# Performance work log

Hardware: AMD Instinct MI355X
Metric: run time of the kernel (lower is better)

Reference implementation:

```python
import jax, jax.numpy as jnp
import numpy as np

DIM = 512
A_HEADS = 8
C_HEADS = 4
DH = 64
EPS = 1e-5


def layer_norm(x, g, b):
    mu = jnp.mean(x, axis=-1, keepdims=True)
    var = jnp.var(x, axis=-1, keepdims=True)
    return (x - mu) * jax.lax.rsqrt(var + EPS) * g + b


def setup_inputs() -> dict:
    key = jax.random.key(0)
    ks = jax.random.split(key, 8)
    inner_a = A_HEADS * DH  # 512
    inner_c = C_HEADS * DH  # 256
    s = 0.02
    return {
        "x": jax.random.normal(ks[0], (4, 192, DIM), dtype=jnp.float32),
        # Attention branch params
        "ln1_g": jnp.ones((DIM,), jnp.float32),
        "ln1_b": jnp.zeros((DIM,), jnp.float32),
        "Wqkv": jax.random.normal(ks[1], (DIM, 3 * inner_a), jnp.float32) * s,
        "Wo": jax.random.normal(ks[2], (inner_a, DIM), jnp.float32) * s,
        "bo": jnp.zeros((DIM,), jnp.float32),
        # Trittention branch params
        "ln2_g": jnp.ones((DIM,), jnp.float32),
        "ln2_b": jnp.zeros((DIM,), jnp.float32),
        "Wabcde": jax.random.normal(ks[3], (DIM, 5 * inner_c), jnp.float32) * s,
        "babcde": jnp.zeros((5 * inner_c,), jnp.float32),
        "Wp": jax.random.normal(ks[4], (inner_c, DIM), jnp.float32) * s,
        "bp": jnp.zeros((DIM,), jnp.float32),
    }


def _attention(x, ln_g, ln_b, Wqkv, Wo, bo):
    B, T, _ = x.shape
    xn = layer_norm(x, ln_g, ln_b)
    qkv = xn @ Wqkv  # [B,T,3*H*D]
    q, k, v = jnp.split(qkv, 3, axis=-1)
    def heads(t):
        return t.reshape(B, T, A_HEADS, DH).transpose(0, 2, 1, 3)  # [B,H,T,D]
    q, k, v = heads(q), heads(k), heads(v)
    scale = DH ** -0.5
    dots = jnp.einsum('bhqd,bhkd->bhqk', q, k) * scale
    attn = jax.nn.softmax(dots, axis=-1)
    out = jnp.einsum('bhqk,bhkd->bhqd', attn, v)
    out = out.transpose(0, 2, 1, 3).reshape(B, T, A_HEADS * DH)
    return out @ Wo + bo


def _trittention(x, ln_g, ln_b, Wabcde, babcde, Wp, bp):
    B, T, _ = x.shape
    xn = layer_norm(x, ln_g, ln_b)
    proj = xn @ Wabcde + babcde  # [B,T,5*H*D]
    a, b_, c, d_, e = jnp.split(proj, 5, axis=-1)
    def heads(t):
        return t.reshape(B, T, C_HEADS, DH)  # [B,T,H,D]
    a, b_, c, d_, e = heads(a), heads(b_), heads(c), heads(d_), heads(e)
    # cubic score: [B,H,S,T,Q]
    score = jnp.einsum('bshd,bthd,bqhd->bhstq', a, b_, c) / DH
    # softmax over joint (s,t) for each query q
    score = score.transpose(0, 1, 4, 2, 3).reshape(B, C_HEADS, T, T * T)
    attn = jax.nn.softmax(score, axis=-1).reshape(B, C_HEADS, T, T, T)
    z = (jnp.einsum('bhqst,bshd->bhqd', attn, d_)
         + jnp.einsum('bhqst,bthd->bhqd', attn, e))
    z = z.transpose(0, 2, 1, 3).reshape(B, T, C_HEADS * DH)
    return z @ Wp + bp


def reference(x, ln1_g, ln1_b, Wqkv, Wo, bo, ln2_g, ln2_b, Wabcde, babcde, Wp, bp):
    return (_attention(x, ln1_g, ln1_b, Wqkv, Wo, bo)
            + _trittention(x, ln2_g, ln2_b, Wabcde, babcde, Wp, bp))
```

## Files before the change

kernel.cpp:

```cpp
#include <hip/hip_runtime.h>
#include <cstdint>


#define B_   4
#define T_   192
#define DIM_ 512
#define AH   8
#define CH   4

typedef unsigned short u16;
typedef unsigned int   u32;
typedef __attribute__((ext_vector_type(8))) short short8;
typedef __attribute__((ext_vector_type(4))) float floatx4;
typedef __attribute__((ext_vector_type(4))) int intx4;
typedef __attribute__((ext_vector_type(2))) float f32x2;
typedef __attribute__((ext_vector_type(8))) _Float16 half8;
typedef __attribute__((ext_vector_type(2))) _Float16 half2v;
typedef __attribute__((ext_vector_type(2))) __fp16 fp16x2;

union Frag  { intx4 i; short8 s; };
union FragH { intx4 i; half8 h; };

__device__ __forceinline__ floatx4 mfma16(Frag a, Frag b, floatx4 c) {
    return __builtin_amdgcn_mfma_f32_16x16x32_bf16(a.s, b.s, c, 0, 0, 0);
}
__device__ __forceinline__ floatx4 mfma16h(FragH a, FragH b, floatx4 c) {
    return __builtin_amdgcn_mfma_f32_16x16x32_f16(a.h, b.h, c, 0, 0, 0);
}

__device__ __forceinline__ float fexp2(float x) {
    return __builtin_amdgcn_exp2f(x);
}

__device__ __forceinline__ float wave_reduce_sum(float v) {
#pragma unroll
    for (int off = 32; off >= 1; off >>= 1)
        v += __shfl_xor(v, off, 64);
    return v;
}

__device__ __forceinline__ u32 pack_rne(float x, float y) {
    u32 ux = __float_as_uint(x);
    u32 uy = __float_as_uint(y);
    ux += 0x7fffu + ((ux >> 16) & 1u);
    uy += 0x7fffu + ((uy >> 16) & 1u);
    return (ux >> 16) | (uy & 0xffff0000u);
}
__device__ __forceinline__ u16 bf16_rne(float x) {
    u32 u = __float_as_uint(x);
    u += 0x7fffu + ((u >> 16) & 1u);
    return (u16)(u >> 16);
}
__device__ __forceinline__ float bf16f(u16 h) { return __uint_as_float(((u32)h) << 16); }

__device__ __forceinline__ u32 pack_f16(float x, float y) {
    union { fp16x2 h; u32 u; } cv;
    cv.h = __builtin_amdgcn_cvt_pkrtz(x, y);
    return cv.u;
}
__device__ __forceinline__ u32 mul_h2(u32 a, u32 b) {
    union { u32 u; half2v h; } ua, ub, uw;
    ua.u = a; ub.u = b;
    uw.h = ua.h * ub.h;
    return uw.u;
}

__device__ __forceinline__ Frag ld_frag8(const u16* p) {
    Frag f;
    uint2 a = *(const uint2*)p;
    uint2 b = *(const uint2*)(p + 4);
    f.i = (intx4){ (int)a.x, (int)a.y, (int)b.x, (int)b.y };
    return f;
}

#define LOG2E 1.44269504088896f

__global__ __launch_bounds__(256) void prep_kernel(
    const float* __restrict__ x,
    const float* __restrict__ g1, const float* __restrict__ b1,
    const float* __restrict__ g2, const float* __restrict__ b2,
    u16* __restrict__ x1h, u16* __restrict__ x2h,
    const float* __restrict__ Wqkv, u16* __restrict__ wqh,
    const float* __restrict__ Wab,  u16* __restrict__ wah,
    const float* __restrict__ Wo,   const float* __restrict__ Wp,
    u16* __restrict__ wofh, float* __restrict__ zero_base, float* __restrict__ outz)
{
    __shared__ union { float t[64][65]; float red[4][2]; } u;
    const int tid = threadIdx.x;
    {
        int gid = blockIdx.x * 256 + tid;
        if (gid < 294912) ((float4*)zero_base)[gid] = make_float4(0.f, 0.f, 0.f, 0.f);
        if (gid < 98304)  ((float4*)outz)[gid]      = make_float4(0.f, 0.f, 0.f, 0.f);
    }
    if (blockIdx.x < 768) {
        int row = blockIdx.x;
        const float2 v = ((const float2*)(x + (size_t)row * DIM_))[tid];
        float s  = v.x + v.y;
        float s2 = v.x * v.x + v.y * v.y;
        s  = wave_reduce_sum(s);
        s2 = wave_reduce_sum(s2);
        int w = tid >> 6;
        if ((tid & 63) == 0) { u.red[w][0] = s; u.red[w][1] = s2; }
        __syncthreads();
        float ts  = u.red[0][0] + u.red[1][0] + u.red[2][0] + u.red[3][0];
        float ts2 = u.red[0][1] + u.red[1][1] + u.red[2][1] + u.red[3][1];
        float mean = ts * (1.0f / DIM_);
        float var  = ts2 * (1.0f / DIM_) - mean * mean;
        float rstd = rsqrtf(var + 1e-5f);
        int c0 = tid * 2;
        float n0 = (v.x - mean) * rstd;
        float n1 = (v.y - mean) * rstd;
        float a0 = n0 * g1[c0] + b1[c0], a1 = n1 * g1[c0 + 1] + b1[c0 + 1];
        float c2 = n0 * g2[c0] + b2[c0], c3 = n1 * g2[c0 + 1] + b2[c0 + 1];
        size_t o = (size_t)row * 256 + tid;
        ((u32*)x1h)[o] = pack_rne(a0, a1);
        ((u32*)x2h)[o] = pack_rne(c2, c3);
        return;
    }
    int id = blockIdx.x - 768;
    const float* W; u16 *H; int K, N, Kout, kofs, tile;
    if (id < 192)      { W = Wqkv; H = wqh;  K = 512; N = 1536; Kout = 512; kofs = 0;   tile = id;       }
    else if (id < 352) { W = Wab;  H = wah;  K = 512; N = 1280; Kout = 512; kofs = 0;   tile = id - 192; }
    else if (id < 416) { W = Wo;   H = wofh; K = 512; N = 512;  Kout = 768; kofs = 0;   tile = id - 352; }
    else               { W = Wp;   H = wofh; K = 256; N = 512;  Kout = 768; kofs = 512; tile = id - 416; }
    int nx = N >> 6;
    int n0 = (tile % nx) * 64, k0 = (tile / nx) * 64;
    int rr = tid >> 4, c4 = (tid & 15) << 2;
#pragma unroll
    for (int p = 0; p < 4; ++p) {
        int row = rr + p * 16;
        float4 v = *(const float4*)(W + (size_t)(k0 + row) * N + n0 + c4);
        u.t[row][c4 + 0] = v.x; u.t[row][c4 + 1] = v.y;
        u.t[row][c4 + 2] = v.z; u.t[row][c4 + 3] = v.w;
    }
    __syncthreads();
#pragma unroll
    for (int p = 0; p < 4; ++p) {
        int n = rr + p * 16;
        u16 hi[4];
#pragma unroll
        for (int c = 0; c < 4; ++c)
            hi[c] = bf16_rne(u.t[c4 + c][n]);
        size_t o = (size_t)(n0 + n) * Kout + kofs + k0 + c4;
        *(uint2*)&H[o] = make_uint2((u32)hi[0] | ((u32)hi[1] << 16), (u32)hi[2] | ((u32)hi[3] << 16));
    }
}

__global__ __launch_bounds__(256) void gemm_dual(
    const u16* __restrict__ x1h, const u16* __restrict__ wqh,
    const u16* __restrict__ x2h, const u16* __restrict__ wah,
    const float* __restrict__ babcde,
    float* __restrict__ qkv, float* __restrict__ proj)
{
    __shared__ u16 As[64][68];
    __shared__ u16 Bs[64][68];
    const int tid = threadIdx.x;
    const int nb = blockIdx.x;
    const u16 *Ah, *BTh; const float* bias; float* C; int N, bn;
    if (nb < 24) { Ah = x1h; BTh = wqh; bias = nullptr; C = qkv;  N = 1536; bn = nb * 64; }
    else         { Ah = x2h; BTh = wah; bias = babcde; C = proj; N = 1280; bn = (nb - 24) * 64; }
    const int K = 512;
    const int bm = blockIdx.y * 64;
    const int lane = tid & 63, wave = tid >> 6;
    const int m16 = lane & 15, quad = lane >> 4;
    const int wm = (wave >> 1) * 32, wn = (wave & 1) * 32;
    const int r = tid >> 2, c16 = (tid & 3) * 16;

    floatx4 acc[2][2];
#pragma unroll
    for (int i = 0; i < 2; ++i)
#pragma unroll
        for (int j = 0; j < 2; ++j) acc[i][j] = (floatx4){0.f, 0.f, 0.f, 0.f};

    for (int k0 = 0; k0 < K; k0 += 64) {
        __syncthreads();
        {
            const u16* pa = Ah + (size_t)(bm + r) * K + k0 + c16;
            uint4 v0 = *(const uint4*)pa, v1 = *(const uint4*)(pa + 8);
            *(uint2*)&As[r][c16 + 0]  = make_uint2(v0.x, v0.y);
            *(uint2*)&As[r][c16 + 4]  = make_uint2(v0.z, v0.w);
            *(uint2*)&As[r][c16 + 8]  = make_uint2(v1.x, v1.y);
            *(uint2*)&As[r][c16 + 12] = make_uint2(v1.z, v1.w);
        }
        {
            const u16* pb = BTh + (size_t)(bn + r) * K + k0 + c16;
            uint4 v0 = *(const uint4*)pb, v1 = *(const uint4*)(pb + 8);
            *(uint2*)&Bs[r][c16 + 0]  = make_uint2(v0.x, v0.y);
            *(uint2*)&Bs[r][c16 + 4]  = make_uint2(v0.z, v0.w);
            *(uint2*)&Bs[r][c16 + 8]  = make_uint2(v1.x, v1.y);
            *(uint2*)&Bs[r][c16 + 12] = make_uint2(v1.z, v1.w);
        }
        __syncthreads();
#pragma unroll
        for (int ks = 0; ks < 2; ++ks) {
            const int ko = ks * 32 + quad * 8;
            Frag a0 = ld_frag8(&As[wm + m16][ko]);
            Frag a1 = ld_frag8(&As[wm + 16 + m16][ko]);
            Frag b0 = ld_frag8(&Bs[wn + m16][ko]);
            Frag b1 = ld_frag8(&Bs[wn + 16 + m16][ko]);
            acc[0][0] = mfma16(a0, b0, acc[0][0]);
            acc[0][1] = mfma16(a0, b1, acc[0][1]);
            acc[1][0] = mfma16(a1, b0, acc[1][0]);
            acc[1][1] = mfma16(a1, b1, acc[1][1]);
        }
    }
#pragma unroll
    for (int i = 0; i < 2; ++i)
#pragma unroll
        for (int rr = 0; rr < 4; ++rr) {
            int m = bm + wm + i * 16 + quad * 4 + rr;
#pragma unroll
            for (int j = 0; j < 2; ++j) {
                int n = bn + wn + j * 16 + m16;
                float v = acc[i][j][rr];
                if (bias) v += bias[n];
                C[(size_t)m * N + n] = v;
            }
        }
}

__global__ __launch_bounds__(256, 3) void attn_tritt(
    const float* __restrict__ qkv, const float* __restrict__ proj,
    u16* __restrict__ aoh, float* __restrict__ rs1, float* __restrict__ rt1)
{
    __shared__ union {
        struct {
            union { u16 Ks[96][68]; u16 P[64][100]; } kp;
            u16 Vt[64][100];
        } at;
        struct {
            u32 a_lds[48 * 36];
            u32 b_lds[48 * 36];
            float rs_lds[48][33];
            float rt_lds[48][33];
        } tr;
    } S;
    const int tid = threadIdx.x;
    const int lane = tid & 63, wave = tid >> 6;
    const int m16 = lane & 15, quad = lane >> 4;

    if (blockIdx.x < 96) {
        const int ab = blockIdx.x;
        const int b = ab / 24, rem = ab % 24;
        const int h = rem / 3, qt3 = rem % 3;
        const int qg = wave;
        const size_t base = (size_t)(b * T_) * 1536 + h * 64;

        Frag qf0, qf1;
        {
            const float s = 0.125f * LOG2E;
            const float* qp = qkv + base + (size_t)(qt3 * 64 + qg * 16 + m16) * 1536 + quad * 8;
            float4 u0 = *(const float4*)qp;
            float4 u1 = *(const float4*)(qp + 4);
            float4 u2 = *(const float4*)(qp + 32);
            float4 u3 = *(const float4*)(qp + 36);
            qf0.i = (intx4){ (int)pack_rne(u0.x * s, u0.y * s), (int)pack_rne(u0.z * s, u0.w * s),
                             (int)pack_rne(u1.x * s, u1.y * s), (int)pack_rne(u1.z * s, u1.w * s) };
            qf1.i = (intx4){ (int)pack_rne(u2.x * s, u2.y * s), (int)pack_rne(u2.z * s, u2.w * s),
                             (int)pack_rne(u3.x * s, u3.y * s), (int)pack_rne(u3.z * s, u3.w * s) };
        }

        float rsum[4] = {0.f, 0.f, 0.f, 0.f};
        floatx4 acco[4];
#pragma unroll
        for (int dt = 0; dt < 4; ++dt) acco[dt] = (floatx4){0.f, 0.f, 0.f, 0.f};

        for (int p = 0; p < 2; ++p) {
            if (p) __syncthreads();
            for (int i = tid; i < 96 * 16; i += 256) {
                int row = i >> 4, c4 = (i & 15) << 2;
                const float* kp = qkv + base + (size_t)(p * 96 + row) * 1536 + 512 + c4;
                float4 kv = *(const float4*)kp;
                *(uint2*)&S.at.kp.Ks[row][c4] = make_uint2(pack_rne(kv.x, kv.y), pack_rne(kv.z, kv.w));
                float4 vv = *(const float4*)(qkv + base + (size_t)(p * 96 + row) * 1536 + 1024 + c4);
                S.at.Vt[c4 + 0][row] = bf16_rne(vv.x);
                S.at.Vt[c4 + 1][row] = bf16_rne(vv.y);
                S.at.Vt[c4 + 2][row] = bf16_rne(vv.z);
                S.at.Vt[c4 + 3][row] = bf16_rne(vv.w);
            }
            __syncthreads();

            float ev[6][4];
#pragma unroll
            for (int tt = 0; tt < 6; ++tt) {
                Frag kb0 = ld_frag8(&S.at.kp.Ks[tt * 16 + m16][quad * 8]);
                Frag kb1 = ld_frag8(&S.at.kp.Ks[tt * 16 + m16][32 + quad * 8]);
                floatx4 accs = (floatx4){0.f, 0.f, 0.f, 0.f};
                accs = mfma16(qf0, kb0, accs);
                accs = mfma16(qf1, kb1, accs);
#pragma unroll
                for (int rr = 0; rr < 4; ++rr) {
                    float e = fexp2(accs[rr]);
                    ev[tt][rr] = e;
                    rsum[rr] += e;
                }
            }
            __syncthreads();
#pragma unroll
            for (int tt = 0; tt < 6; ++tt)
#pragma unroll
                for (int rr = 0; rr < 4; ++rr)
                    S.at.kp.P[qg * 16 + quad * 4 + rr][tt * 16 + m16] = bf16_rne(ev[tt][rr]);
#pragma unroll
            for (int ts = 0; ts < 3; ++ts) {
                Frag pf = ld_frag8(&S.at.kp.P[qg * 16 + m16][ts * 32 + quad * 8]);
#pragma unroll
                for (int dt = 0; dt < 4; ++dt) {
                    Frag vf = ld_frag8(&S.at.Vt[dt * 16 + m16][ts * 32 + quad * 8]);
                    acco[dt] = mfma16(pf, vf, acco[dt]);
                }
            }
        }

        float rinv[4];
#pragma unroll
        for (int rr = 0; rr < 4; ++rr) {
            float v = rsum[rr];
            v += __shfl_xor(v, 1, 64);
            v += __shfl_xor(v, 2, 64);
            v += __shfl_xor(v, 4, 64);
            v += __shfl_xor(v, 8, 64);
            rinv[rr] = 1.0f / v;
        }
#pragma unroll
        for (int dt = 0; dt < 4; ++dt)
#pragma unroll
            for (int rr = 0; rr < 4; ++rr) {
                float o = acco[dt][rr] * rinv[rr];
                size_t idx = (size_t)(b * T_ + qt3 * 64 + qg * 16 + quad * 4 + rr) * 512
                           + h * 64 + dt * 16 + m16;
                aoh[idx] = bf16_rne(o);
            }
        return;
    }

    const int t2 = blockIdx.x - 96;
    const int xx = t2 % 96;
    const int h = (t2 / 96) % CH;
    const int b = t2 / (96 * CH);
    const int qt = xx >> 4;
    const int sc = (xx >> 2) & 3;
    const int tc = xx & 3;
    const int q0 = qt * 32, s0 = sc * 48, t0 = tc * 48;
    const int bh = b * CH + h;
    const size_t rowbase = (size_t)(b * T_) * 1280 + h * 64;
    const float kA = 0.015625f * LOG2E;

    for (int i = tid; i < 48 * 32; i += 256) {
        int row = i >> 5, cp = i & 31;
        const float2 va = *(const float2*)(proj + rowbase + (size_t)(s0 + row) * 1280 + 0 + cp * 2);
        S.tr.a_lds[row * 36 + cp] = pack_f16(va.x * kA, va.y * kA);
        const float2 vb = *(const float2*)(proj + rowbase + (size_t)(t0 + row) * 1280 + 256 + cp * 2);
        S.tr.b_lds[row * 36 + cp] = pack_f16(vb.x, vb.y);
    }

    FragH cf[2][2];
#pragma unroll
    for (int jq = 0; jq < 2; ++jq) {
        const float* cp = proj + rowbase + (size_t)(q0 + jq * 16 + m16) * 1280 + 512 + quad * 8;
        float4 u0 = *(const float4*)(cp);
        float4 u1 = *(const float4*)(cp + 4);
        float4 u2 = *(const float4*)(cp + 32);
        float4 u3 = *(const float4*)(cp + 36);
        cf[jq][0].i = (intx4){ (int)pack_f16(u0.x, u0.y), (int)pack_f16(u0.z, u0.w),
                               (int)pack_f16(u1.x, u1.y), (int)pack_f16(u1.z, u1.w) };
        cf[jq][1].i = (intx4){ (int)pack_f16(u2.x, u2.y), (int)pack_f16(u2.z, u2.w),
                               (int)pack_f16(u3.x, u3.y), (int)pack_f16(u3.z, u3.w) };
    }
    __syncthreads();

    float rt_acc[3][4][2] = {};

    for (int si = 0; si < 12; ++si) {
        const int srow = wave * 12 + si;
        const intx4 av0 = *(const intx4*)(S.tr.a_lds + srow * 36 + quad * 4);
        const intx4 av1 = *(const intx4*)(S.tr.a_lds + srow * 36 + 16 + quad * 4);
        float rs_s[2] = {0.f, 0.f};
#pragma unroll
        for (int tt = 0; tt < 3; ++tt) {
            const u32* bp2 = S.tr.b_lds + (tt * 16 + m16) * 36;
            intx4 bv0 = *(const intx4*)(bp2 + quad * 4);
            intx4 bv1 = *(const intx4*)(bp2 + 16 + quad * 4);
            FragH w0, w1;
#pragma unroll
            for (int j = 0; j < 4; ++j) {
                w0.i[j] = (int)mul_h2((u32)av0[j], (u32)bv0[j]);
                w1.i[j] = (int)mul_h2((u32)av1[j], (u32)bv1[j]);
            }
#pragma unroll
            for (int jq = 0; jq < 2; ++jq) {
                floatx4 acc = (floatx4){0.f, 0.f, 0.f, 0.f};
                acc = mfma16h(w0, cf[jq][0], acc);
                acc = mfma16h(w1, cf[jq][1], acc);
#pragma unroll
                for (int rr = 0; rr < 4; ++rr) {
                    float e = fexp2(acc[rr]);
                    rt_acc[tt][rr][jq] += e;
                    rs_s[jq] += e;
                }
            }
        }
#pragma unroll
        for (int jq = 0; jq < 2; ++jq) {
            float v = rs_s[jq];
            v += __shfl_xor(v, 16, 64);
            v += __shfl_xor(v, 32, 64);
            if (lane < 16) S.tr.rs_lds[srow][jq * 16 + m16] = v;
        }
    }

    __syncthreads();
    for (int w = 0; w < 4; ++w) {
        if (wave == w) {
#pragma unroll
            for (int tt = 0; tt < 3; ++tt)
#pragma unroll
                for (int rr = 0; rr < 4; ++rr) {
                    int t = tt * 16 + quad * 4 + rr;
#pragma unroll
                    for (int jq = 0; jq < 2; ++jq) {
                        if (w == 0) S.tr.rt_lds[t][jq * 16 + m16] = rt_acc[tt][rr][jq];
                        else        S.tr.rt_lds[t][jq * 16 + m16] += rt_acc[tt][rr][jq];
                    }
                }
        }
        __syncthreads();
    }
    for (int i = tid; i < 32 * 48; i += 256) {
        int qq = i / 48, ss = i - qq * 48;
        unsafeAtomicAdd(&rs1[((size_t)bh * T_ + q0 + qq) * T_ + s0 + ss], S.tr.rs_lds[ss][qq]);
    }
    for (int i = tid; i < 32 * 48; i += 256) {
        int qq = i / 48, t3 = i - qq * 48;
        unsafeAtomicAdd(&rt1[((size_t)bh * T_ + q0 + qq) * T_ + t0 + t3], S.tr.rt_lds[t3][qq]);
    }
}

__global__ __launch_bounds__(256) void finale(
    const u16* __restrict__ aoh, const float* __restrict__ rs1, const float* __restrict__ rt1,
    const float* __restrict__ proj, const u16* __restrict__ wofh,
    const float* __restrict__ bo, const float* __restrict__ bp,
    float* __restrict__ out)
{
    __shared__ union {
        struct { u16 As[32][68]; u16 Bs[64][68]; } A;
        struct { u16 Am[2][32][68]; u16 Bs[64][68]; float zred[32][9]; float Zl[32]; } B;
    } S;
    const int tid = threadIdx.x;
    const int lane = tid & 63, wave = tid >> 6;
    const int m16 = lane & 15, quad = lane >> 4;

    if (blockIdx.x < 192) {
        const int bn = (blockIdx.x & 7) * 64, bm = (blockIdx.x >> 3) * 32;
        const int wm = (wave >> 1) * 16, wn = (wave & 1) * 32;
        const int ra = tid >> 3, c8 = (tid & 7) * 8;
        const int rb = tid >> 2, c16 = (tid & 3) * 16;

        floatx4 acc[2];
        acc[0] = (floatx4){0.f, 0.f, 0.f, 0.f};
        acc[1] = (floatx4){0.f, 0.f, 0.f, 0.f};

        for (int k0 = 0; k0 < 512; k0 += 64) {
            __syncthreads();
            {
                const u16* pah = aoh + (size_t)(bm + ra) * 512 + k0 + c8;
                uint4 v = *(const uint4*)pah;
                *(uint2*)&S.A.As[ra][c8 + 0] = make_uint2(v.x, v.y);
                *(uint2*)&S.A.As[ra][c8 + 4] = make_uint2(v.z, v.w);
            }
            {
                const u16* pb = wofh + (size_t)(bn + rb) * 768 + k0 + c16;
                uint4 v0 = *(const uint4*)pb, v1 = *(const uint4*)(pb + 8);
                *(uint2*)&S.A.Bs[rb][c16 + 0]  = make_uint2(v0.x, v0.y);
                *(uint2*)&S.A.Bs[rb][c16 + 4]  = make_uint2(v0.z, v0.w);
                *(uint2*)&S.A.Bs[rb][c16 + 8]  = make_uint2(v1.x, v1.y);
                *(uint2*)&S.A.Bs[rb][c16 + 12] = make_uint2(v1.z, v1.w);
            }
            __syncthreads();
#pragma unroll
            for (int ks = 0; ks < 2; ++ks) {
                const int ko = ks * 32 + quad * 8;
                Frag ah = ld_frag8(&S.A.As[wm + m16][ko]);
                Frag b0 = ld_frag8(&S.A.Bs[wn + m16][ko]);
                Frag b1 = ld_frag8(&S.A.Bs[wn + 16 + m16][ko]);
                acc[0] = mfma16(ah, b0, acc[0]);
                acc[1] = mfma16(ah, b1, acc[1]);
            }
        }
#pragma unroll
        for (int rr = 0; rr < 4; ++rr) {
            int m = bm + wm + quad * 4 + rr;
#pragma unroll
            for (int j = 0; j < 2; ++j) {
                int n = bn + wn + j * 16 + m16;
                unsafeAtomicAdd(&out[(size_t)m * 512 + n], acc[j][rr] + bo[n] + bp[n]);
            }
        }
        return;
    }

    const int blockB = blockIdx.x - 192;
    const int mt = blockB % 6, bh = blockB / 6;
    const int b = bh >> 2, h = bh & 3;
    const int q0 = mt * 32;
    const int wm = (wave >> 1) * 16, wn = (wave & 1) * 32;
    const int ra = tid >> 3, c8 = (tid & 7) * 8;
    const int sl = tid >> 2, d4b = (tid & 3) * 4;

    float zacc = 0.f;
    floatx4 acc[2];
    acc[0] = (floatx4){0.f, 0.f, 0.f, 0.f};
    acc[1] = (floatx4){0.f, 0.f, 0.f, 0.f};

    for (int k0 = 0; k0 < 384; k0 += 64) {
        __syncthreads();
        {
            float g[8];
            if (k0 < 192) {
                const float* p = rs1 + ((size_t)bh * T_ + q0 + ra) * T_ + k0 + c8;
                float4 v0 = *(const float4*)(p);
                float4 v1 = *(const float4*)(p + 4);
                g[0] = v0.x; g[1] = v0.y; g[2] = v0.z; g[3] = v0.w;
                g[4] = v1.x; g[5] = v1.y; g[6] = v1.z; g[7] = v1.w;
                zacc += ((g[0] + g[1]) + (g[2] + g[3])) + ((g[4] + g[5]) + (g[6] + g[7]));
            } else {
                const float* p = rt1 + ((size_t)bh * T_ + q0 + ra) * T_ + (k0 - 192) + c8;
                float4 v0 = *(const float4*)(p);
                float4 v1 = *(const float4*)(p + 4);
                g[0] = v0.x; g[1] = v0.y; g[2] = v0.z; g[3] = v0.w;
                g[4] = v1.x; g[5] = v1.y; g[6] = v1.z; g[7] = v1.w;
            }
#pragma unroll
            for (int i = 0; i < 8; ++i) {
                u16 hi = bf16_rne(g[i]);
                S.B.Am[0][ra][c8 + i] = hi;
                S.B.Am[1][ra][c8 + i] = bf16_rne(g[i] - bf16f(hi));
            }
        }
        {
            const int colbase = (k0 < 192 ? 768 : 1024) + h * 64;
            const int s0 = (k0 < 192 ? k0 : k0 - 192);
#pragma unroll
            for (int i = 0; i < 4; ++i) {
                int dd = d4b + i * 16;
                float4 v = *(const float4*)(proj + (size_t)(b * T_ + s0 + sl) * 1280 + colbase + dd);
                S.B.Bs[dd + 0][sl] = bf16_rne(v.x);
                S.B.Bs[dd + 1][sl] = bf16_rne(v.y);
                S.B.Bs[dd + 2][sl] = bf16_rne(v.z);
                S.B.Bs[dd + 3][sl] = bf16_rne(v.w);
            }
        }
        __syncthreads();
#pragma unroll
        for (int ks = 0; ks < 2; ++ks) {
            const int ko = ks * 32 + quad * 8;
            Frag gh = ld_frag8(&S.B.Am[0][wm + m16][ko]);
            Frag gl = ld_frag8(&S.B.Am[1][wm + m16][ko]);
            Frag d0 = ld_frag8(&S.B.Bs[wn + m16][ko]);
            Frag d1 = ld_frag8(&S.B.Bs[wn + 16 + m16][ko]);
            acc[0] = mfma16(gh, d0, acc[0]);
            acc[0] = mfma16(gl, d0, acc[0]);
            acc[1] = mfma16(gh, d1, acc[1]);
            acc[1] = mfma16(gl, d1, acc[1]);
        }
    }
    S.B.zred[ra][tid & 7] = zacc;
    __syncthreads();
    if (tid < 32) {
        float s = ((S.B.zred[tid][0] + S.B.zred[tid][1]) + (S.B.zred[tid][2] + S.B.zred[tid][3]))
                + ((S.B.zred[tid][4] + S.B.zred[tid][5]) + (S.B.zred[tid][6] + S.B.zred[tid][7]));
        S.B.Zl[tid] = 1.0f / s;
    }
    __syncthreads();
    {
        float zv[2][4];
#pragma unroll
        for (int j = 0; j < 2; ++j)
#pragma unroll
            for (int rr = 0; rr < 4; ++rr) {
                int m = wm + quad * 4 + rr;
                zv[j][rr] = acc[j][rr] * S.B.Zl[m];
            }
        __syncthreads();
#pragma unroll
        for (int j = 0; j < 2; ++j)
#pragma unroll
            for (int rr = 0; rr < 4; ++rr) {
                int m = wm + quad * 4 + rr;
                int d = wn + j * 16 + m16;
                S.B.Am[0][m][d] = bf16_rne(zv[j][rr]);
            }
    }
    __syncthreads();
#pragma unroll
    for (int t = 0; t < 8; ++t) {
        const int n0 = wave * 128 + t * 16;
        Frag bf0 = ld_frag8(&wofh[(size_t)(n0 + m16) * 768 + 512 + h * 64 + quad * 8]);
        Frag bf1 = ld_frag8(&wofh[(size_t)(n0 + m16) * 768 + 512 + h * 64 + 32 + quad * 8]);
#pragma unroll
        for (int qi = 0; qi < 2; ++qi) {
            Frag za = ld_frag8(&S.B.Am[0][qi * 16 + m16][quad * 8]);
            Frag zb = ld_frag8(&S.B.Am[0][qi * 16 + m16][32 + quad * 8]);
            floatx4 ac = (floatx4){0.f, 0.f, 0.f, 0.f};
            ac = mfma16(za, bf0, ac);
            ac = mfma16(zb, bf1, ac);
#pragma unroll
            for (int rr = 0; rr < 4; ++rr) {
                int m = b * T_ + q0 + qi * 16 + quad * 4 + rr;
                unsafeAtomicAdd(&out[(size_t)m * 512 + n0 + m16], ac[rr]);
            }
        }
    }
}

extern "C" void kernel_launch(void* const* d_in, const int* in_sizes, int n_in,
                              void* d_out, int out_size, void* d_ws, size_t ws_size,
                              hipStream_t stream)
{
    const float* x      = (const float*)d_in[0];
    const float* ln1_g  = (const float*)d_in[1];
    const float* ln1_b  = (const float*)d_in[2];
    const float* Wqkv   = (const float*)d_in[3];
    const float* Wo     = (const float*)d_in[4];
    const float* bo     = (const float*)d_in[5];
    const float* ln2_g  = (const float*)d_in[6];
    const float* ln2_b  = (const float*)d_in[7];
    const float* Wabcde = (const float*)d_in[8];
    const float* babcde = (const float*)d_in[9];
    const float* Wp     = (const float*)d_in[10];
    const float* bp     = (const float*)d_in[11];
    float* out = (float*)d_out;

    float* ws   = (float*)d_ws;
    float* proj = ws;
    u16* wofh   = (u16*)(ws + 983040);
    u16* aoh    = (u16*)(ws + 1179648);
    float* qkv  = ws + 1376256;
    u16* x1h    = (u16*)(ws + 2555904);
    u16* x2h    = (u16*)(ws + 2752512);
    u16* wqh    = (u16*)(ws + 2949120);
    u16* wah    = (u16*)(ws + 3342336);
    float* rs1  = ws + 3670016;
    float* rt1  = ws + 4259840;

    prep_kernel<<<1216, 256, 0, stream>>>(x, ln1_g, ln1_b, ln2_g, ln2_b,
                                          x1h, x2h,
                                          Wqkv, wqh, Wabcde, wah,
                                          Wo, Wp, wofh, rs1, out);
    gemm_dual<<<dim3(44, 12), 256, 0, stream>>>(x1h, wqh, x2h, wah,
                                                babcde, qkv, proj);
    attn_tritt<<<96 + 1536, 256, 0, stream>>>(qkv, proj, aoh, rs1, rt1);
    finale<<<288, 256, 0, stream>>>(aoh, rs1, rt1, proj, wofh, bo, bp, out);
}
```

Baseline: 139.7 us.

## Fuse four kernel launches into one persistent kernel with grid barriers

Replaces the prep, dual GEMM, attention/trittention and finale launches with a single persistent kernel of 544 blocks. Each block loops over virtual block ids for every phase, and an atomic-counter grid barrier separates the phases. This removes launch overhead and the idle gaps between kernels, at the cost of an extra memset, spin-wait barriers, and a shared-memory union that may lower occupancy. It also requires all 544 blocks to be co-resident, or the barrier deadlocks.

```diff
diff --git a/kernel.cpp b/kernel.cpp
--- a/kernel.cpp
+++ b/kernel.cpp
@@ -74,540 +74,535 @@
 }
 
 #define LOG2E 1.44269504088896f
-
-__global__ __launch_bounds__(256) void prep_kernel(
+#define GRID_ 544
+
+__device__ __forceinline__ void gridbar(u32* bar, u32 target) {
+    __syncthreads();
+    if (threadIdx.x == 0) {
+        __threadfence();
+        atomicAdd(bar, 1u);
+        while (atomicAdd(bar, 0u) < target)
+            __builtin_amdgcn_s_sleep(8);
+        __threadfence();
+    }
+    __syncthreads();
+}
+
+__global__ __launch_bounds__(256, 4) void mega(
     const float* __restrict__ x,
     const float* __restrict__ g1, const float* __restrict__ b1,
     const float* __restrict__ g2, const float* __restrict__ b2,
-    u16* __restrict__ x1h, u16* __restrict__ x2h,
-    const float* __restrict__ Wqkv, u16* __restrict__ wqh,
-    const float* __restrict__ Wab,  u16* __restrict__ wah,
+    const float* __restrict__ Wqkv, const float* __restrict__ Wab,
     const float* __restrict__ Wo,   const float* __restrict__ Wp,
-    u16* __restrict__ wofh, float* __restrict__ zero_base, float* __restrict__ outz)
-{
-    __shared__ union { float t[64][65]; float red[4][2]; } u;
-    const int tid = threadIdx.x;
-    {
-        int gid = blockIdx.x * 256 + tid;
-        if (gid < 294912) ((float4*)zero_base)[gid] = make_float4(0.f, 0.f, 0.f, 0.f);
-        if (gid < 98304)  ((float4*)outz)[gid]      = make_float4(0.f, 0.f, 0.f, 0.f);
-    }
-    if (blockIdx.x < 768) {
-        int row = blockIdx.x;
-        const float2 v = ((const float2*)(x + (size_t)row * DIM_))[tid];
-        float s  = v.x + v.y;
-        float s2 = v.x * v.x + v.y * v.y;
-        s  = wave_reduce_sum(s);
-        s2 = wave_reduce_sum(s2);
-        int w = tid >> 6;
-        if ((tid & 63) == 0) { u.red[w][0] = s; u.red[w][1] = s2; }
-        __syncthreads();
-        float ts  = u.red[0][0] + u.red[1][0] + u.red[2][0] + u.red[3][0];
-        float ts2 = u.red[0][1] + u.red[1][1] + u.red[2][1] + u.red[3][1];
-        float mean = ts * (1.0f / DIM_);
-        float var  = ts2 * (1.0f / DIM_) - mean * mean;
-        float rstd = rsqrtf(var + 1e-5f);
-        int c0 = tid * 2;
-        float n0 = (v.x - mean) * rstd;
-        float n1 = (v.y - mean) * rstd;
-        float a0 = n0 * g1[c0] + b1[c0], a1 = n1 * g1[c0 + 1] + b1[c0 + 1];
-        float c2 = n0 * g2[c0] + b2[c0], c3 = n1 * g2[c0 + 1] + b2[c0 + 1];
-        size_t o = (size_t)row * 256 + tid;
-        ((u32*)x1h)[o] = pack_rne(a0, a1);
-        ((u32*)x2h)[o] = pack_rne(c2, c3);
-        return;
-    }
-    int id = blockIdx.x - 768;
-    const float* W; u16 *H; int K, N, Kout, kofs, tile;
-    if (id < 192)      { W = Wqkv; H = wqh;  K = 512; N = 1536; Kout = 512; kofs = 0;   tile = id;       }
-    else if (id < 352) { W = Wab;  H = wah;  K = 512; N = 1280; Kout = 512; kofs = 0;   tile = id - 192; }
-    else if (id < 416) { W = Wo;   H = wofh; K = 512; N = 512;  Kout = 768; kofs = 0;   tile = id - 352; }
-    else               { W = Wp;   H = wofh; K = 256; N = 512;  Kout = 768; kofs = 512; tile = id - 416; }
-    int nx = N >> 6;
-    int n0 = (tile % nx) * 64, k0 = (tile / nx) * 64;
-    int rr = tid >> 4, c4 = (tid & 15) << 2;
-#pragma unroll
-    for (int p = 0; p < 4; ++p) {
-        int row = rr + p * 16;
-        float4 v = *(const float4*)(W + (size_t)(k0 + row) * N + n0 + c4);
-        u.t[row][c4 + 0] = v.x; u.t[row][c4 + 1] = v.y;
-        u.t[row][c4 + 2] = v.z; u.t[row][c4 + 3] = v.w;
-    }
-    __syncthreads();
-#pragma unroll
-    for (int p = 0; p < 4; ++p) {
-        int n = rr + p * 16;
-        u16 hi[4];
-#pragma unroll
-        for (int c = 0; c < 4; ++c)
-            hi[c] = bf16_rne(u.t[c4 + c][n]);
-        size_t o = (size_t)(n0 + n) * Kout + kofs + k0 + c4;
-        *(uint2*)&H[o] = make_uint2((u32)hi[0] | ((u32)hi[1] << 16), (u32)hi[2] | ((u32)hi[3] << 16));
-    }
-}
-
-__global__ __launch_bounds__(256) void gemm_dual(
-    const u16* __restrict__ x1h, const u16* __restrict__ wqh,
-    const u16* __restrict__ x2h, const u16* __restrict__ wah,
     const float* __restrict__ babcde,
-    float* __restrict__ qkv, float* __restrict__ proj)
-{
-    __shared__ u16 As[64][68];
-    __shared__ u16 Bs[64][68];
-    const int tid = threadIdx.x;
-    const int nb = blockIdx.x;
-    const u16 *Ah, *BTh; const float* bias; float* C; int N, bn;
-    if (nb < 24) { Ah = x1h; BTh = wqh; bias = nullptr; C = qkv;  N = 1536; bn = nb * 64; }
-    else         { Ah = x2h; BTh = wah; bias = babcde; C = proj; N = 1280; bn = (nb - 24) * 64; }
-    const int K = 512;
-    const int bm = blockIdx.y * 64;
-    const int lane = tid & 63, wave = tid >> 6;
-    const int m16 = lane & 15, quad = lane >> 4;
-    const int wm = (wave >> 1) * 32, wn = (wave & 1) * 32;
-    const int r = tid >> 2, c16 = (tid & 3) * 16;
-
-    floatx4 acc[2][2];
-#pragma unroll
-    for (int i = 0; i < 2; ++i)
-#pragma unroll
-        for (int j = 0; j < 2; ++j) acc[i][j] = (floatx4){0.f, 0.f, 0.f, 0.f};
-
-    for (int k0 = 0; k0 < K; k0 += 64) {
-        __syncthreads();
-        {
-            const u16* pa = Ah + (size_t)(bm + r) * K + k0 + c16;
-            uint4 v0 = *(const uint4*)pa, v1 = *(const uint4*)(pa + 8);
-            *(uint2*)&As[r][c16 + 0]  = make_uint2(v0.x, v0.y);
-            *(uint2*)&As[r][c16 + 4]  = make_uint2(v0.z, v0.w);
-            *(uint2*)&As[r][c16 + 8]  = make_uint2(v1.x, v1.y);
-            *(uint2*)&As[r][c16 + 12] = make_uint2(v1.z, v1.w);
-        }
-        {
-            const u16* pb = BTh + (size_t)(bn + r) * K + k0 + c16;
-            uint4 v0 = *(const uint4*)pb, v1 = *(const uint4*)(pb + 8);
-            *(uint2*)&Bs[r][c16 + 0]  = make_uint2(v0.x, v0.y);
-            *(uint2*)&Bs[r][c16 + 4]  = make_uint2(v0.z, v0.w);
-            *(uint2*)&Bs[r][c16 + 8]  = make_uint2(v1.x, v1.y);
-            *(uint2*)&Bs[r][c16 + 12] = make_uint2(v1.z, v1.w);
-        }
-        __syncthreads();
-#pragma unroll
-        for (int ks = 0; ks < 2; ++ks) {
-            const int ko = ks * 32 + quad * 8;
-            Frag a0 = ld_frag8(&As[wm + m16][ko]);
-            Frag a1 = ld_frag8(&As[wm + 16 + m16][ko]);
-            Frag b0 = ld_frag8(&Bs[wn + m16][ko]);
-            Frag b1 = ld_frag8(&Bs[wn + 16 + m16][ko]);
-            acc[0][0] = mfma16(a0, b0, acc[0][0]);
-            acc[0][1] = mfma16(a0, b1, acc[0][1]);
-            acc[1][0] = mfma16(a1, b0, acc[1][0]);
-            acc[1][1] = mfma16(a1, b1, acc[1][1]);
-        }
-    }
-#pragma unroll
-    for (int i = 0; i < 2; ++i)
-#pragma unroll
-        for (int rr = 0; rr < 4; ++rr) {
-            int m = bm + wm + i * 16 + quad * 4 + rr;
-#pragma unroll
-            for (int j = 0; j < 2; ++j) {
-                int n = bn + wn + j * 16 + m16;
-                float v = acc[i][j][rr];
-                if (bias) v += bias[n];
-                C[(size_t)m * N + n] = v;
-            }
-        }
-}
-
-__global__ __launch_bounds__(256, 3) void attn_tritt(
-    const float* __restrict__ qkv, const float* __restrict__ proj,
-    u16* __restrict__ aoh, float* __restrict__ rs1, float* __restrict__ rt1)
+    const float* __restrict__ bo, const float* __restrict__ bp,
+    float* __restrict__ proj, u16* __restrict__ wofh, u16* __restrict__ aoh,
+    float* __restrict__ qkv, u16* __restrict__ x1h, u16* __restrict__ x2h,
+    u16* __restrict__ wqh, u16* __restrict__ wah,
+    float* __restrict__ rs1, float* __restrict__ rt1,
+    u32* __restrict__ bar,
+    float* __restrict__ out)
 {
     __shared__ union {
-        struct {
-            union { u16 Ks[96][68]; u16 P[64][100]; } kp;
-            u16 Vt[64][100];
-        } at;
-        struct {
-            u32 a_lds[48 * 36];
-            u32 b_lds[48 * 36];
-            float rs_lds[48][33];
-            float rt_lds[48][33];
-        } tr;
+        union { float t[64][65]; float red[4][2]; } pr;
+        struct { u16 As[64][68]; u16 Bs[64][68]; } gd;
+        struct { union { u16 Ks[96][68]; u16 P[64][100]; } kp; u16 Vt[64][100]; } at;
+        struct { u32 a_lds[48 * 36]; u32 b_lds[48 * 36];
+                 float rs_lds[48][33]; float rt_lds[48][33]; } tr;
+        struct { u16 As[32][68]; u16 Bs[64][68]; } fA;
+        struct { u16 Am[2][32][68]; u16 Bs[64][68]; float zred[32][9]; float Zl[32]; } fB;
     } S;
     const int tid = threadIdx.x;
     const int lane = tid & 63, wave = tid >> 6;
     const int m16 = lane & 15, quad = lane >> 4;
 
-    if (blockIdx.x < 96) {
-        const int ab = blockIdx.x;
-        const int b = ab / 24, rem = ab % 24;
-        const int h = rem / 3, qt3 = rem % 3;
-        const int qg = wave;
-        const size_t base = (size_t)(b * T_) * 1536 + h * 64;
-
-        Frag qf0, qf1;
+    for (int vb = blockIdx.x; vb < 1216; vb += GRID_) {
+        __syncthreads();
         {
-            const float s = 0.125f * LOG2E;
-            const float* qp = qkv + base + (size_t)(qt3 * 64 + qg * 16 + m16) * 1536 + quad * 8;
-            float4 u0 = *(const float4*)qp;
-            float4 u1 = *(const float4*)(qp + 4);
-            float4 u2 = *(const float4*)(qp + 32);
-            float4 u3 = *(const float4*)(qp + 36);
-            qf0.i = (intx4){ (int)pack_rne(u0.x * s, u0.y * s), (int)pack_rne(u0.z * s, u0.w * s),
-                             (int)pack_rne(u1.x * s, u1.y * s), (int)pack_rne(u1.z * s, u1.w * s) };
-            qf1.i = (intx4){ (int)pack_rne(u2.x * s, u2.y * s), (int)pack_rne(u2.z * s, u2.w * s),
-                             (int)pack_rne(u3.x * s, u3.y * s), (int)pack_rne(u3.z * s, u3.w * s) };
+            int gid = vb * 256 + tid;
+            if (gid < 294912) ((float4*)rs1)[gid] = make_float4(0.f, 0.f, 0.f, 0.f);
+            if (gid < 98304)  ((float4*)out)[gid] = make_float4(0.f, 0.f, 0.f, 0.f);
         }
-
-        float rsum[4] = {0.f, 0.f, 0.f, 0.f};
-        floatx4 acco[4];
-#pragma unroll
-        for (int dt = 0; dt < 4; ++dt) acco[dt] = (floatx4){0.f, 0.f, 0.f, 0.f};
-
-        for (int p = 0; p < 2; ++p) {
-            if (p) __syncthreads();
-            for (int i = tid; i < 96 * 16; i += 256) {
-                int row = i >> 4, c4 = (i & 15) << 2;
-                const float* kp = qkv + base + (size_t)(p * 96 + row) * 1536 + 512 + c4;
-                float4 kv = *(const float4*)kp;
-                *(uint2*)&S.at.kp.Ks[row][c4] = make_uint2(pack_rne(kv.x, kv.y), pack_rne(kv.z, kv.w));
-                float4 vv = *(const float4*)(qkv + base + (size_t)(p * 96 + row) * 1536 + 1024 + c4);
-                S.at.Vt[c4 + 0][row] = bf16_rne(vv.x);
-                S.at.Vt[c4 + 1][row] = bf16_rne(vv.y);
-                S.at.Vt[c4 + 2][row] = bf16_rne(vv.z);
-                S.at.Vt[c4 + 3][row] = bf16_rne(vv.w);
-            }
-            __syncthreads();
-
-            float ev[6][4];
-#pragma unroll
-            for (int tt = 0; tt < 6; ++tt) {
-                Frag kb0 = ld_frag8(&S.at.kp.Ks[tt * 16 + m16][quad * 8]);
-                Frag kb1 = ld_frag8(&S.at.kp.Ks[tt * 16 + m16][32 + quad * 8]);
-                floatx4 accs = (floatx4){0.f, 0.f, 0.f, 0.f};
-                accs = mfma16(qf0, kb0, accs);
-                accs = mfma16(qf1, kb1, accs);
-#pragma unroll
-                for (int rr = 0; rr < 4; ++rr) {
-                    float e = fexp2(accs[rr]);
-                    ev[tt][rr] = e;
-                    rsum[rr] += e;
-                }
-            }
-            __syncthreads();
-#pragma unroll
-            for (int tt = 0; tt < 6; ++tt)
-#pragma unroll
-                for (int rr = 0; rr < 4; ++rr)
-                    S.at.kp.P[qg * 16 + quad * 4 + rr][tt * 16 + m16] = bf16_rne(ev[tt][rr]);
-#pragma unroll
-            for (int ts = 0; ts < 3; ++ts) {
-                Frag pf = ld_frag8(&S.at.kp.P[qg * 16 + m16][ts * 32 + quad * 8]);
-#pragma unroll
-                for (int dt = 0; dt < 4; ++dt) {
-                    Frag vf = ld_frag8(&S.at.Vt[dt * 16 + m16][ts * 32 + quad * 8]);
-                    acco[dt] = mfma16(pf, vf, acco[dt]);
-                }
-            }
-        }
-
-        float rinv[4];
-#pragma unroll
-        for (int rr = 0; rr < 4; ++rr) {
-            float v = rsum[rr];
-            v += __shfl_xor(v, 1, 64);
-            v += __shfl_xor(v, 2, 64);
-            v += __shfl_xor(v, 4, 64);
-            v += __shfl_xor(v, 8, 64);
-            rinv[rr] = 1.0f / v;
-        }
-#pragma unroll
-        for (int dt = 0; dt < 4; ++dt)
-#pragma unroll
-            for (int rr = 0; rr < 4; ++rr) {
-                float o = acco[dt][rr] * rinv[rr];
-                size_t idx = (size_t)(b * T_ + qt3 * 64 + qg * 16 + quad * 4 + rr) * 512
-                           + h * 64 + dt * 16 + m16;
-                aoh[idx] = bf16_rne(o);
-            }
-        return;
-    }
-
-    const int t2 = blockIdx.x - 96;
-    const int xx = t2 % 96;
-    const int h = (t2 / 96) % CH;
-    const int b = t2 / (96 * CH);
-    const int qt = xx >> 4;
-    const int sc = (xx >> 2) & 3;
-    const int tc = xx & 3;
-    const int q0 = qt * 32, s0 = sc * 48, t0 = tc * 48;
-    const int bh = b * CH + h;
-    const size_t rowbase = (size_t)(b * T_) * 1280 + h * 64;
-    const float kA = 0.015625f * LOG2E;
-
-    for (int i = tid; i < 48 * 32; i += 256) {
-        int row = i >> 5, cp = i & 31;
-        const float2 va = *(const float2*)(proj + rowbase + (size_t)(s0 + row) * 1280 + 0 + cp * 2);
-        S.tr.a_lds[row * 36 + cp] = pack_f16(va.x * kA, va.y * kA);
-        const float2 vb = *(const float2*)(proj + rowbase + (size_t)(t0 + row) * 1280 + 256 + cp * 2);
-        S.tr.b_lds[row * 36 + cp] = pack_f16(vb.x, vb.y);
-    }
-
-    FragH cf[2][2];
-#pragma unroll
-    for (int jq = 0; jq < 2; ++jq) {
-        const float* cp = proj + rowbase + (size_t)(q0 + jq * 16 + m16) * 1280 + 512 + quad * 8;
-        float4 u0 = *(const float4*)(cp);
-        float4 u1 = *(const float4*)(cp + 4);
-        float4 u2 = *(const float4*)(cp + 32);
-        float4 u3 = *(const float4*)(cp + 36);
-        cf[jq][0].i = (intx4){ (int)pack_f16(u0.x, u0.y), (int)pack_f16(u0.z, u0.w),
-                               (int)pack_f16(u1.x, u1.y), (int)pack_f16(u1.z, u1.w) };
-        cf[jq][1].i = (intx4){ (int)pack_f16(u2.x, u2.y), (int)pack_f16(u2.z, u2.w),
-                               (int)pack_f16(u3.x, u3.y), (int)pack_f16(u3.z, u3.w) };
-    }
-    __syncthreads();
-
-    float rt_acc[3][4][2] = {};
-
-    for (int si = 0; si < 12; ++si) {
-        const int srow = wave * 12 + si;
-        const intx4 av0 = *(const intx4*)(S.tr.a_lds + srow * 36 + quad * 4);
-        const intx4 av1 = *(const intx4*)(S.tr.a_lds + srow * 36 + 16 + quad * 4);
-        float rs_s[2] = {0.f, 0.f};
-#pragma unroll
-        for (int tt = 0; tt < 3; ++tt) {
-            const u32* bp2 = S.tr.b_lds + (tt * 16 + m16) * 36;
-            intx4 bv0 = *(const intx4*)(bp2 + quad * 4);
-            intx4 bv1 = *(const intx4*)(bp2 + 16 + quad * 4);
-            FragH w0, w1;
-#pragma unroll
-            for (int j = 0; j < 4; ++j) {
-                w0.i[j] = (int)mul_h2((u32)av0[j], (u32)bv0[j]);
-                w1.i[j] = (int)mul_h2((u32)av1[j], (u32)bv1[j]);
-            }
-#pragma unroll
-            for (int jq = 0; jq < 2; ++jq) {
-                floatx4 acc = (floatx4){0.f, 0.f, 0.f, 0.f};
-                acc = mfma16h(w0, cf[jq][0], acc);
-                acc = mfma16h(w1, cf[jq][1], acc);
-#pragma unroll
-                for (int rr = 0; rr < 4; ++rr) {
-                    float e = fexp2(acc[rr]);
-                    rt_acc[tt][rr][jq] += e;
-                    rs_s[jq] += e;
-                }
-            }
-        }
-#pragma unroll
-        for (int jq = 0; jq < 2; ++jq) {
-            float v = rs_s[jq];
-            v += __shfl_xor(v, 16, 64);
-            v += __shfl_xor(v, 32, 64);
-            if (lane < 16) S.tr.rs_lds[srow][jq * 16 + m16] = v;
+        if (vb < 768) {
+            int row = vb;
+            const float2 v = ((const float2*)(x + (size_t)row * DIM_))[tid];
+            float s  = v.x + v.y;
+            float s2 = v.x * v.x + v.y * v.y;
+            s  = wave_reduce_sum(s);
+            s2 = wave_reduce_sum(s2);
+            int w = tid >> 6;
+            if ((tid & 63) == 0) { S.pr.red[w][0] = s; S.pr.red[w][1] = s2; }
+            __syncthreads();
+            float ts  = S.pr.red[0][0] + S.pr.red[1][0] + S.pr.red[2][0] + S.pr.red[3][0];
+            float ts2 = S.pr.red[0][1] + S.pr.red[1][1] + S.pr.red[2][1] + S.pr.red[3][1];
+            float mean = ts * (1.0f / DIM_);
+            float var  = ts2 * (1.0f / DIM_) - mean * mean;
+            float rstd = rsqrtf(var + 1e-5f);
+            int c0 = tid * 2;
+            float n0 = (v.x - mean) * rstd;
+            float n1 = (v.y - mean) * rstd;
+            float a0 = n0 * g1[c0] + b1[c0], a1 = n1 * g1[c0 + 1] + b1[c0 + 1];
+            float c2 = n0 * g2[c0] + b2[c0], c3 = n1 * g2[c0 + 1] + b2[c0 + 1];
+            size_t o = (size_t)row * 256 + tid;
+            ((u32*)x1h)[o] = pack_rne(a0, a1);
+            ((u32*)x2h)[o] = pack_rne(c2, c3);
+        } else {
+            int id = vb - 768;
+            const float* W; u16 *H; int K, N, Kout, kofs, tile;
+            if (id < 192)      { W = Wqkv; H = wqh;  K = 512; N = 1536; Kout = 512; kofs = 0;   tile = id;       }
+            else if (id < 352) { W = Wab;  H = wah;  K = 512; N = 1280; Kout = 512; kofs = 0;   tile = id - 192; }
+            else if (id < 416) { W = Wo;   H = wofh; K = 512; N = 512;  Kout = 768; kofs = 0;   tile = id - 352; }
+            else               { W = Wp;   H = wofh; K = 256; N = 512;  Kout = 768; kofs = 512; tile = id - 416; }
+            int nx = N >> 6;
+            int n0 = (tile % nx) * 64, k0 = (tile / nx) * 64;
+            int rr = tid >> 4, c4 = (tid & 15) << 2;
+#pragma unroll
+            for (int p = 0; p < 4; ++p) {
+                int row = rr + p * 16;
+                float4 v = *(const float4*)(W + (size_t)(k0 + row) * N + n0 + c4);
+                S.pr.t[row][c4 + 0] = v.x; S.pr.t[row][c4 + 1] = v.y;
+                S.pr.t[row][c4 + 2] = v.z; S.pr.t[row][c4 + 3] = v.w;
+            }
+            __syncthreads();
+#pragma unroll
+            for (int p = 0; p < 4; ++p) {
+                int n = rr + p * 16;
+                u16 hi[4];
+#pragma unroll
+                for (int c = 0; c < 4; ++c)
+                    hi[c] = bf16_rne(S.pr.t[c4 + c][n]);
+                size_t o = (size_t)(n0 + n) * Kout + kofs + k0 + c4;
+                *(uint2*)&H[o] = make_uint2((u32)hi[0] | ((u32)hi[1] << 16),
+                                            (u32)hi[2] | ((u32)hi[3] << 16));
+            }
         }
     }
-
-    __syncthreads();
-    for (int w = 0; w < 4; ++w) {
-        if (wave == w) {
-#pragma unroll
-            for (int tt = 0; tt < 3; ++tt)
-#pragma unroll
-                for (int rr = 0; rr < 4; ++rr) {
-                    int t = tt * 16 + quad * 4 + rr;
-#pragma unroll
-                    for (int jq = 0; jq < 2; ++jq) {
-                        if (w == 0) S.tr.rt_lds[t][jq * 16 + m16] = rt_acc[tt][rr][jq];
-                        else        S.tr.rt_lds[t][jq * 16 + m16] += rt_acc[tt][rr][jq];
-                    }
-                }
+    gridbar(bar, GRID_);
+
+    for (int vb = blockIdx.x; vb < 528; vb += GRID_) {
+        const int nb = vb % 44;
+        const int bm = (vb / 44) * 64;
+        const u16 *Ah, *BTh; const float* bias; float* C; int N, bn;
+        if (nb < 24) { Ah = x1h; BTh = wqh; bias = nullptr; C = qkv;  N = 1536; bn = nb * 64; }
+        else         { Ah = x2h; BTh = wah; bias = babcde; C = proj; N = 1280; bn = (nb - 24) * 64; }
+        const int K = 512;
+        const int wm = (wave >> 1) * 32, wn = (wave & 1) * 32;
+        const int r = tid >> 2, c16 = (tid & 3) * 16;
+
+        floatx4 acc[2][2];
+#pragma unroll
+        for (int i = 0; i < 2; ++i)
+#pragma unroll
+            for (int j = 0; j < 2; ++j) acc[i][j] = (floatx4){0.f, 0.f, 0.f, 0.f};
+
+        for (int k0 = 0; k0 < K; k0 += 64) {
+            __syncthreads();
+            {
+                const u16* pa = Ah + (size_t)(bm + r) * K + k0 + c16;
+                uint4 v0 = *(const uint4*)pa, v1 = *(const uint4*)(pa + 8);
+                *(uint2*)&S.gd.As[r][c16 + 0]  = make_uint2(v0.x, v0.y);
+                *(uint2*)&S.gd.As[r][c16 + 4]  = make_uint2(v0.z, v0.w);
+                *(uint2*)&S.gd.As[r][c16 + 8]  = make_uint2(v1.x, v1.y);
+                *(uint2*)&S.gd.As[r][c16 + 12] = make_uint2(v1.z, v1.w);
+            }
+            {
+                const u16* pb = BTh + (size_t)(bn + r) * K + k0 + c16;
+                uint4 v0 = *(const uint4*)pb, v1 = *(const uint4*)(pb + 8);
+                *(uint2*)&S.gd.Bs[r][c16 + 0]  = make_uint2(v0.x, v0.y);
+                *(uint2*)&S.gd.Bs[r][c16 + 4]  = make_uint2(v0.z, v0.w);
+                *(uint2*)&S.gd.Bs[r][c16 + 8]  = make_uint2(v1.x, v1.y);
+                *(uint2*)&S.gd.Bs[r][c16 + 12] = make_uint2(v1.z, v1.w);
+            }
+            __syncthreads();
+#pragma unroll
+            for (int ks = 0; ks < 2; ++ks) {
+                const int ko = ks * 32 + quad * 8;
+                Frag a0 = ld_frag8(&S.gd.As[wm + m16][ko]);
+                Frag a1 = ld_frag8(&S.gd.As[wm + 16 + m16][ko]);
+                Frag b0 = ld_frag8(&S.gd.Bs[wn + m16][ko]);
+                Frag b1 = ld_frag8(&S.gd.Bs[wn + 16 + m16][ko]);
+                acc[0][0] = mfma16(a0, b0, acc[0][0]);
+                acc[0][1] = mfma16(a0, b1, acc[0][1]);
+                acc[1][0] = mfma16(a1, b0, acc[1][0]);
+                acc[1][1] = mfma16(a1, b1, acc[1][1]);
+            }
         }
+#pragma unroll
+        for (int i = 0; i < 2; ++i)
+#pragma unroll
+            for (int rr = 0; rr < 4; ++rr) {
+                int m = bm + wm + i * 16 + quad * 4 + rr;
+#pragma unroll
+                for (int j = 0; j < 2; ++j) {
+                    int n = bn + wn + j * 16 + m16;
+                    float v = acc[i][j][rr];
+                    if (bias) v += bias[n];
+                    C[(size_t)m * N + n] = v;
+                }
+            }
         __syncthreads();
     }
-    for (int i = tid; i < 32 * 48; i += 256) {
-        int qq = i / 48, ss = i - qq * 48;
-        unsafeAtomicAdd(&rs1[((size_t)bh * T_ + q0 + qq) * T_ + s0 + ss], S.tr.rs_lds[ss][qq]);
-    }
-    for (int i = tid; i < 32 * 48; i += 256) {
-        int qq = i / 48, t3 = i - qq * 48;
-        unsafeAtomicAdd(&rt1[((size_t)bh * T_ + q0 + qq) * T_ + t0 + t3], S.tr.rt_lds[t3][qq]);
-    }
-}
-
-__global__ __launch_bounds__(256) void finale(
-    const u16* __restrict__ aoh, const float* __restrict__ rs1, const float* __restrict__ rt1,
-    const float* __restrict__ proj, const u16* __restrict__ wofh,
-    const float* __restrict__ bo, const float* __restrict__ bp,
-    float* __restrict__ out)
-{
-    __shared__ union {
-        struct { u16 As[32][68]; u16 Bs[64][68]; } A;
-        struct { u16 Am[2][32][68]; u16 Bs[64][68]; float zred[32][9]; float Zl[32]; } B;
-    } S;
-    const int tid = threadIdx.x;
-    const int lane = tid & 63, wave = tid >> 6;
-    const int m16 = lane & 15, quad = lane >> 4;
-
-    if (blockIdx.x < 192) {
-        const int bn = (blockIdx.x & 7) * 64, bm = (blockIdx.x >> 3) * 32;
-        const int wm = (wave >> 1) * 16, wn = (wave & 1) * 32;
-        const int ra = tid >> 3, c8 = (tid & 7) * 8;
-        const int rb = tid >> 2, c16 = (tid & 3) * 16;
-
-        floatx4 acc[2];
-        acc[0] = (floatx4){0.f, 0.f, 0.f, 0.f};
-        acc[1] = (floatx4){0.f, 0.f, 0.f, 0.f};
-
-        for (int k0 = 0; k0 < 512; k0 += 64) {
-            __syncthreads();
+    gridbar(bar, 2 * GRID_);
+
+    for (int vb = blockIdx.x; vb < 1632; vb += GRID_) {
+        __syncthreads();
+        if (vb < 96) {
+            const int ab = vb;
+            const int b = ab / 24, rem = ab % 24;
+            const int h = rem / 3, qt3 = rem % 3;
+            const int qg = wave;
+            const size_t base = (size_t)(b * T_) * 1536 + h * 64;
+
+            Frag qf0, qf1;
             {
-                const u16* pah = aoh + (size_t)(bm + ra) * 512 + k0 + c8;
-                uint4 v = *(const uint4*)pah;
-                *(uint2*)&S.A.As[ra][c8 + 0] = make_uint2(v.x, v.y);
-                *(uint2*)&S.A.As[ra][c8 + 4] = make_uint2(v.z, v.w);
-            }
-            {
-                const u16* pb = wofh + (size_t)(bn + rb) * 768 + k0 + c16;
-                uint4 v0 = *(const uint4*)pb, v1 = *(const uint4*)(pb + 8);
-                *(uint2*)&S.A.Bs[rb][c16 + 0]  = make_uint2(v0.x, v0.y);
-                *(uint2*)&S.A.Bs[rb][c16 + 4]  = make_uint2(v0.z, v0.w);
-                *(uint2*)&S.A.Bs[rb][c16 + 8]  = make_uint2(v1.x, v1.y);
-                *(uint2*)&S.A.Bs[rb][c16 + 12] = make_uint2(v1.z, v1.w);
-            }
-            __syncthreads();
-#pragma unroll
-            for (int ks = 0; ks < 2; ++ks) {
-                const int ko = ks * 32 + quad * 8;
-                Frag ah = ld_frag8(&S.A.As[wm + m16][ko]);
-                Frag b0 = ld_frag8(&S.A.Bs[wn + m16][ko]);
-                Frag b1 = ld_frag8(&S.A.Bs[wn + 16 + m16][ko]);
-                acc[0] = mfma16(ah, b0, acc[0]);
-                acc[1] = mfma16(ah, b1, acc[1]);
-            }
-        }
-#pragma unroll
-        for (int rr = 0; rr < 4; ++rr) {
-            int m = bm + wm + quad * 4 + rr;
-#pragma unroll
-            for (int j = 0; j < 2; ++j) {
-                int n = bn + wn + j * 16 + m16;
-                unsafeAtomicAdd(&out[(size_t)m * 512 + n], acc[j][rr] + bo[n] + bp[n]);
-            }
-        }
-        return;
-    }
-
-    const int blockB = blockIdx.x - 192;
-    const int mt = blockB % 6, bh = blockB / 6;
-    const int b = bh >> 2, h = bh & 3;
-    const int q0 = mt * 32;
-    const int wm = (wave >> 1) * 16, wn = (wave & 1) * 32;
-    const int ra = tid >> 3, c8 = (tid & 7) * 8;
-    const int sl = tid >> 2, d4b = (tid & 3) * 4;
-
-    float zacc = 0.f;
-    floatx4 acc[2];
-    acc[0] = (floatx4){0.f, 0.f, 0.f, 0.f};
-    acc[1] = (floatx4){0.f, 0.f, 0.f, 0.f};
-
-    for (int k0 = 0; k0 < 384; k0 += 64) {
-        __syncthreads();
-        {
-            float g[8];
-            if (k0 < 192) {
-                const float* p = rs1 + ((size_t)bh * T_ + q0 + ra) * T_ + k0 + c8;
-                float4 v0 = *(const float4*)(p);
-                float4 v1 = *(const float4*)(p + 4);
-                g[0] = v0.x; g[1] = v0.y; g[2] = v0.z; g[3] = v0.w;
-                g[4] = v1.x; g[5] = v1.y; g[6] = v1.z; g[7] = v1.w;
-                zacc += ((g[0] + g[1]) + (g[2] + g[3])) + ((g[4] + g[5]) + (g[6] + g[7]));
-            } else {
-                const float* p = rt1 + ((size_t)bh * T_ + q0 + ra) * T_ + (k0 - 192) + c8;
-                float4 v0 = *(const float4*)(p);
-                float4 v1 = *(const float4*)(p + 4);
-                g[0] = v0.x; g[1] = v0.y; g[2] = v0.z; g[3] = v0.w;
-                g[4] = v1.x; g[5] = v1.y; g[6] = v1.z; g[7] = v1.w;
-            }
-#pragma unroll
-            for (int i = 0; i < 8; ++i) {
-                u16 hi = bf16_rne(g[i]);
-                S.B.Am[0][ra][c8 + i] = hi;
-                S.B.Am[1][ra][c8 + i] = bf16_rne(g[i] - bf16f(hi));
-            }
-        }
-        {
-            const int colbase = (k0 < 192 ? 768 : 1024) + h * 64;
-            const int s0 = (k0 < 192 ? k0 : k0 - 192);
-#pragma unroll
-            for (int i = 0; i < 4; ++i) {
-                int dd = d4b + i * 16;
-                float4 v = *(const float4*)(proj + (size_t)(b * T_ + s0 + sl) * 1280 + colbase + dd);
-                S.B.Bs[dd + 0][sl] = bf16_rne(v.x);
-                S.B.Bs[dd + 1][sl] = bf16_rne(v.y);
-                S.B.Bs[dd + 2][sl] = bf16_rne(v.z);
-                S.B.Bs[dd + 3][sl] = bf16_rne(v.w);
-            }
-        }
-        __syncthreads();
-#pragma unroll
-        for (int ks = 0; ks < 2; ++ks) {
-            const int ko = ks * 32 + quad * 8;
-            Frag gh = ld_frag8(&S.B.Am[0][wm + m16][ko]);
-            Frag gl = ld_frag8(&S.B.Am[1][wm + m16][ko]);
-            Frag d0 = ld_frag8(&S.B.Bs[wn + m16][ko]);
-            Frag d1 = ld_frag8(&S.B.Bs[wn + 16 + m16][ko]);
-            acc[0] = mfma16(gh, d0, acc[0]);
-            acc[0] = mfma16(gl, d0, acc[0]);
-            acc[1] = mfma16(gh, d1, acc[1]);
-            acc[1] = mfma16(gl, d1, acc[1]);
+                const float s = 0.125f * LOG2E;
+                const float* qp = qkv + base + (size_t)(qt3 * 64 + qg * 16 + m16) * 1536 + quad * 8;
+                float4 u0 = *(const float4*)qp;
+                float4 u1 = *(const float4*)(qp + 4);
+                float4 u2 = *(const float4*)(qp + 32);
+                float4 u3 = *(const float4*)(qp + 36);
+                qf0.i = (intx4){ (int)pack_rne(u0.x * s, u0.y * s), (int)pack_rne(u0.z * s, u0.w * s),
+                                 (int)pack_rne(u1.x * s, u1.y * s), (int)pack_rne(u1.z * s, u1.w * s) };
+                qf1.i = (intx4){ (int)pack_rne(u2.x * s, u2.y * s), (int)pack_rne(u2.z * s, u2.w * s),
+                                 (int)pack_rne(u3.x * s, u3.y * s), (int)pack_rne(u3.z * s, u3.w * s) };
+            }
+
+            float rsum[4] = {0.f, 0.f, 0.f, 0.f};
+            floatx4 acco[4];
+#pragma unroll
+            for (int dt = 0; dt < 4; ++dt) acco[dt] = (floatx4){0.f, 0.f, 0.f, 0.f};
+
+            for (int p = 0; p < 2; ++p) {
+                if (p) __syncthreads();
+                for (int i = tid; i < 96 * 16; i += 256) {
+                    int row = i >> 4, c4 = (i & 15) << 2;
+                    const float* kp = qkv + base + (size_t)(p * 96 + row) * 1536 + 512 + c4;
+                    float4 kv = *(const float4*)kp;
+                    *(uint2*)&S.at.kp.Ks[row][c4] = make_uint2(pack_rne(kv.x, kv.y), pack_rne(kv.z, kv.w));
+                    float4 vv = *(const float4*)(qkv + base + (size_t)(p * 96 + row) * 1536 + 1024 + c4);
+                    S.at.Vt[c4 + 0][row] = bf16_rne(vv.x);
+                    S.at.Vt[c4 + 1][row] = bf16_rne(vv.y);
+                    S.at.Vt[c4 + 2][row] = bf16_rne(vv.z);
+                    S.at.Vt[c4 + 3][row] = bf16_rne(vv.w);
+                }
+                __syncthreads();
+
+                float ev[6][4];
+#pragma unroll
+                for (int tt = 0; tt < 6; ++tt) {
+                    Frag kb0 = ld_frag8(&S.at.kp.Ks[tt * 16 + m16][quad * 8]);
+                    Frag kb1 = ld_frag8(&S.at.kp.Ks[tt * 16 + m16][32 + quad * 8]);
+                    floatx4 accs = (floatx4){0.f, 0.f, 0.f, 0.f};
+                    accs = mfma16(qf0, kb0, accs);
+                    accs = mfma16(qf1, kb1, accs);
+#pragma unroll
+                    for (int rr = 0; rr < 4; ++rr) {
+                        float e = fexp2(accs[rr]);
+                        ev[tt][rr] = e;
+                        rsum[rr] += e;
+                    }
+                }
+                __syncthreads();
+#pragma unroll
+                for (int tt = 0; tt < 6; ++tt)
+#pragma unroll
+                    for (int rr = 0; rr < 4; ++rr)
+                        S.at.kp.P[qg * 16 + quad * 4 + rr][tt * 16 + m16] = bf16_rne(ev[tt][rr]);
+#pragma unroll
+                for (int ts = 0; ts < 3; ++ts) {
+                    Frag pf = ld_frag8(&S.at.kp.P[qg * 16 + m16][ts * 32 + quad * 8]);
+#pragma unroll
+                    for (int dt = 0; dt < 4; ++dt) {
+                        Frag vf = ld_frag8(&S.at.Vt[dt * 16 + m16][ts * 32 + quad * 8]);
+                        acco[dt] = mfma16(pf, vf, acco[dt]);
+                    }
+                }
+            }
+
+            float rinv[4];
+#pragma unroll
+            for (int rr = 0; rr < 4; ++rr) {
+                float v = rsum[rr];
+                v += __shfl_xor(v, 1, 64);
+                v += __shfl_xor(v, 2, 64);
+                v += __shfl_xor(v, 4, 64);
+                v += __shfl_xor(v, 8, 64);
+                rinv[rr] = 1.0f / v;
+            }
+#pragma unroll
+            for (int dt = 0; dt < 4; ++dt)
+#pragma unroll
+                for (int rr = 0; rr < 4; ++rr) {
+                    float o = acco[dt][rr] * rinv[rr];
+                    size_t idx = (size_t)(b * T_ + qt3 * 64 + qg * 16 + quad * 4 + rr) * 512
+                               + h * 64 + dt * 16 + m16;
+                    aoh[idx] = bf16_rne(o);
+                }
+        } else {
+            const int t2 = vb - 96;
+            const int xx = t2 % 96;
+            const int h = (t2 / 96) % CH;
+            const int b = t2 / (96 * CH);
+            const int qt = xx >> 4;
+            const int sc = (xx >> 2) & 3;
+            const int tc = xx & 3;
+            const int q0 = qt * 32, s0 = sc * 48, t0 = tc * 48;
+            const int bh = b * CH + h;
+            const size_t rowbase = (size_t)(b * T_) * 1280 + h * 64;
+            const float kA = 0.015625f * LOG2E;
+
+            for (int i = tid; i < 48 * 32; i += 256) {
+                int row = i >> 5, cp = i & 31;
+                const float2 va = *(const float2*)(proj + rowbase + (size_t)(s0 + row) * 1280 + 0 + cp * 2);
+                S.tr.a_lds[row * 36 + cp] = pack_f16(va.x * kA, va.y * kA);
+                const float2 vb2 = *(const float2*)(proj + rowbase + (size_t)(t0 + row) * 1280 + 256 + cp * 2);
+                S.tr.b_lds[row * 36 + cp] = pack_f16(vb2.x, vb2.y);
+            }
+
+            FragH cf[2][2];
+#pragma unroll
+            for (int jq = 0; jq < 2; ++jq) {
+                const float* cp = proj + rowbase + (size_t)(q0 + jq * 16 + m16) * 1280 + 512 + quad * 8;
+                float4 u0 = *(const float4*)(cp);
+                float4 u1 = *(const float4*)(cp + 4);
+                float4 u2 = *(const float4*)(cp + 32);
+                float4 u3 = *(const float4*)(cp + 36);
+                cf[jq][0].i = (intx4){ (int)pack_f16(u0.x, u0.y), (int)pack_f16(u0.z, u0.w),
+                                       (int)pack_f16(u1.x, u1.y), (int)pack_f16(u1.z, u1.w) };
+                cf[jq][1].i = (intx4){ (int)pack_f16(u2.x, u2.y), (int)pack_f16(u2.z, u2.w),
+                                       (int)pack_f16(u3.x, u3.y), (int)pack_f16(u3.z, u3.w) };
+            }
+            __syncthreads();
+
+            float rt_acc[3][4][2] = {};
+
+            for (int si = 0; si < 12; ++si) {
+                const int srow = wave * 12 + si;
+                const intx4 av0 = *(const intx4*)(S.tr.a_lds + srow * 36 + quad * 4);
+                const intx4 av1 = *(const intx4*)(S.tr.a_lds + srow * 36 + 16 + quad * 4);
+                float rs_s[2] = {0.f, 0.f};
+#pragma unroll
+                for (int tt = 0; tt < 3; ++tt) {
+                    const u32* bp2 = S.tr.b_lds + (tt * 16 + m16) * 36;
+                    intx4 bv0 = *(const intx4*)(bp2 + quad * 4);
+                    intx4 bv1 = *(const intx4*)(bp2 + 16 + quad * 4);
+                    FragH w0, w1;
+#pragma unroll
+                    for (int j = 0; j < 4; ++j) {
+                        w0.i[j] = (int)mul_h2((u32)av0[j], (u32)bv0[j]);
+                        w1.i[j] = (int)mul_h2((u32)av1[j], (u32)bv1[j]);
+                    }
+#pragma unroll
+                    for (int jq = 0; jq < 2; ++jq) {
+                        floatx4 acc = (floatx4){0.f, 0.f, 0.f, 0.f};
+                        acc = mfma16h(w0, cf[jq][0], acc);
+                        acc = mfma16h(w1, cf[jq][1], acc);
+#pragma unroll
+                        for (int rr = 0; rr < 4; ++rr) {
+                            float e = fexp2(acc[rr]);
+                            rt_acc[tt][rr][jq] += e;
+                            rs_s[jq] += e;
+                        }
+                    }
+                }
+#pragma unroll
+                for (int jq = 0; jq < 2; ++jq) {
+                    float v = rs_s[jq];
+                    v += __shfl_xor(v, 16, 64);
+                    v += __shfl_xor(v, 32, 64);
+                    if (lane < 16) S.tr.rs_lds[srow][jq * 16 + m16] = v;
+                }
+            }
+
+            __syncthreads();
+            for (int w = 0; w < 4; ++w) {
+                if (wave == w) {
+#pragma unroll
+                    for (int tt = 0; tt < 3; ++tt)
+#pragma unroll
+                        for (int rr = 0; rr < 4; ++rr) {
+                            int t = tt * 16 + quad * 4 + rr;
+#pragma unroll
+                            for (int jq = 0; jq < 2; ++jq) {
+                                if (w == 0) S.tr.rt_lds[t][jq * 16 + m16] = rt_acc[tt][rr][jq];
+                                else        S.tr.rt_lds[t][jq * 16 + m16] += rt_acc[tt][rr][jq];
+                            }
+                        }
+                }
+                __syncthreads();
+            }
+            for (int i = tid; i < 32 * 48; i += 256) {
+                int qq = i / 48, ss = i - qq * 48;
+                unsafeAtomicAdd(&rs1[((size_t)bh * T_ + q0 + qq) * T_ + s0 + ss], S.tr.rs_lds[ss][qq]);
+            }
+            for (int i = tid; i < 32 * 48; i += 256) {
+                int qq = i / 48, t3 = i - qq * 48;
+                unsafeAtomicAdd(&rt1[((size_t)bh * T_ + q0 + qq) * T_ + t0 + t3], S.tr.rt_lds[t3][qq]);
+            }
         }
     }
-    S.B.zred[ra][tid & 7] = zacc;
-    __syncthreads();
-    if (tid < 32) {
-        float s = ((S.B.zred[tid][0] + S.B.zred[tid][1]) + (S.B.zred[tid][2] + S.B.zred[tid][3]))
-                + ((S.B.zred[tid][4] + S.B.zred[tid][5]) + (S.B.zred[tid][6] + S.B.zred[tid][7]));
-        S.B.Zl[tid] = 1.0f / s;
-    }
-    __syncthreads();
-    {
-        float zv[2][4];
-#pragma unroll
-        for (int j = 0; j < 2; ++j)
+    gridbar(bar, 3 * GRID_);
+
+    for (int vb = blockIdx.x; vb < 288; vb += GRID_) {
+        __syncthreads();
+        if (vb < 192) {
+            const int bn = (vb & 7) * 64, bm = (vb >> 3) * 32;
+            const int wm = (wave >> 1) * 16, wn = (wave & 1) * 32;
+            const int ra = tid >> 3, c8 = (tid & 7) * 8;
+            const int rb = tid >> 2, c16 = (tid & 3) * 16;
+
+            floatx4 acc[2];
+            acc[0] = (floatx4){0.f, 0.f, 0.f, 0.f};
+            acc[1] = (floatx4){0.f, 0.f, 0.f, 0.f};
+
+            for (int k0 = 0; k0 < 512; k0 += 64) {
+                __syncthreads();
+                {
+                    const u16* pah = aoh + (size_t)(bm + ra) * 512 + k0 + c8;
+                    uint4 v = *(const uint4*)pah;
+                    *(uint2*)&S.fA.As[ra][c8 + 0] = make_uint2(v.x, v.y);
+                    *(uint2*)&S.fA.As[ra][c8 + 4] = make_uint2(v.z, v.w);
+                }
+                {
+                    const u16* pb = wofh + (size_t)(bn + rb) * 768 + k0 + c16;
+                    uint4 v0 = *(const uint4*)pb, v1 = *(const uint4*)(pb + 8);
+                    *(uint2*)&S.fA.Bs[rb][c16 + 0]  = make_uint2(v0.x, v0.y);
+                    *(uint2*)&S.fA.Bs[rb][c16 + 4]  = make_uint2(v0.z, v0.w);
+                    *(uint2*)&S.fA.Bs[rb][c16 + 8]  = make_uint2(v1.x, v1.y);
+                    *(uint2*)&S.fA.Bs[rb][c16 + 12] = make_uint2(v1.z, v1.w);
+                }
+                __syncthreads();
+#pragma unroll
+                for (int ks = 0; ks < 2; ++ks) {
+                    const int ko = ks * 32 + quad * 8;
+                    Frag ah = ld_frag8(&S.fA.As[wm + m16][ko]);
+                    Frag b0 = ld_frag8(&S.fA.Bs[wn + m16][ko]);
+                    Frag b1 = ld_frag8(&S.fA.Bs[wn + 16 + m16][ko]);
+                    acc[0] = mfma16(ah, b0, acc[0]);
+                    acc[1] = mfma16(ah, b1, acc[1]);
+                }
+            }
 #pragma unroll
             for (int rr = 0; rr < 4; ++rr) {
-                int m = wm + quad * 4 + rr;
-                zv[j][rr] = acc[j][rr] * S.B.Zl[m];
-            }
-        __syncthreads();
-#pragma unroll
-        for (int j = 0; j < 2; ++j)
-#pragma unroll
-            for (int rr = 0; rr < 4; ++rr) {
-                int m = wm + quad * 4 + rr;
-                int d = wn + j * 16 + m16;
-                S.B.Am[0][m][d] = bf16_rne(zv[j][rr]);
-            }
-    }
-    __syncthreads();
-#pragma unroll
-    for (int t = 0; t < 8; ++t) {
-        const int n0 = wave * 128 + t * 16;
-        Frag bf0 = ld_frag8(&wofh[(size_t)(n0 + m16) * 768 + 512 + h * 64 + quad * 8]);
-        Frag bf1 = ld_frag8(&wofh[(size_t)(n0 + m16) * 768 + 512 + h * 64 + 32 + quad * 8]);
-#pragma unroll
-        for (int qi = 0; qi < 2; ++qi) {
-            Frag za = ld_frag8(&S.B.Am[0][qi * 16 + m16][quad * 8]);
-            Frag zb = ld_frag8(&S.B.Am[0][qi * 16 + m16][32 + quad * 8]);
-            floatx4 ac = (floatx4){0.f, 0.f, 0.f, 0.f};
-            ac = mfma16(za, bf0, ac);
-            ac = mfma16(zb, bf1, ac);
-#pragma unroll
-            for (int rr = 0; rr < 4; ++rr) {
-                int m = b * T_ + q0 + qi * 16 + quad * 4 + rr;
-                unsafeAtomicAdd(&out[(size_t)m * 512 + n0 + m16], ac[rr]);
+                int m = bm + wm + quad * 4 + rr;
+#pragma unroll
+                for (int j = 0; j < 2; ++j) {
+                    int n = bn + wn + j * 16 + m16;
+                    unsafeAtomicAdd(&out[(size_t)m * 512 + n], acc[j][rr] + bo[n] + bp[n]);
+                }
+            }
+        } else {
+            const int blockB = vb - 192;
+            const int mt = blockB % 6, bh = blockB / 6;
+            const int b = bh >> 2, h = bh & 3;
+            const int q0 = mt * 32;
+            const int wm = (wave >> 1) * 16, wn = (wave & 1) * 32;
+            const int ra = tid >> 3, c8 = (tid & 7) * 8;
+            const int sl = tid >> 2, d4b = (tid & 3) * 4;
+
+            float zacc = 0.f;
+            floatx4 acc[2];
+            acc[0] = (floatx4){0.f, 0.f, 0.f, 0.f};
+            acc[1] = (floatx4){0.f, 0.f, 0.f, 0.f};
+
+            for (int k0 = 0; k0 < 384; k0 += 64) {
+                __syncthreads();
+                {
+                    float g[8];
+                    if (k0 < 192) {
+                        const float* p = rs1 + ((size_t)bh * T_ + q0 + ra) * T_ + k0 + c8;
+                        float4 v0 = *(const float4*)(p);
+                        float4 v1 = *(const float4*)(p + 4);
+                        g[0] = v0.x; g[1] = v0.y; g[2] = v0.z; g[3] = v0.w;
+                        g[4] = v1.x; g[5] = v1.y; g[6] = v1.z; g[7] = v1.w;
+                        zacc += ((g[0] + g[1]) + (g[2] + g[3])) + ((g[4] + g[5]) + (g[6] + g[7]));
+                    } else {
+                        const float* p = rt1 + ((size_t)bh * T_ + q0 + ra) * T_ + (k0 - 192) + c8;
+                        float4 v0 = *(const float4*)(p);
+                        float4 v1 = *(const float4*)(p + 4);
+                        g[0] = v0.x; g[1] = v0.y; g[2] = v0.z; g[3] = v0.w;
+                        g[4] = v1.x; g[5] = v1.y; g[6] = v1.z; g[7] = v1.w;
+                    }
+#pragma unroll
+                    for (int i = 0; i < 8; ++i) {
+                        u16 hi = bf16_rne(g[i]);
+                        S.fB.Am[0][ra][c8 + i] = hi;
+                        S.fB.Am[1][ra][c8 + i] = bf16_rne(g[i] - bf16f(hi));
+                    }
+                }
+                {
+                    const int colbase = (k0 < 192 ? 768 : 1024) + h * 64;
+                    const int s0 = (k0 < 192 ? k0 : k0 - 192);
+#pragma unroll
+                    for (int i = 0; i < 4; ++i) {
+                        int dd = d4b + i * 16;
+                        float4 v = *(const float4*)(proj + (size_t)(b * T_ + s0 + sl) * 1280 + colbase + dd);
+                        S.fB.Bs[dd + 0][sl] = bf16_rne(v.x);
+                        S.fB.Bs[dd + 1][sl] = bf16_rne(v.y);
+                        S.fB.Bs[dd + 2][sl] = bf16_rne(v.z);
+                        S.fB.Bs[dd + 3][sl] = bf16_rne(v.w);
+                    }
+                }
+                __syncthreads();
+#pragma unroll
+                for (int ks = 0; ks < 2; ++ks) {
+                    const int ko = ks * 32 + quad * 8;
+                    Frag gh = ld_frag8(&S.fB.Am[0][wm + m16][ko]);
+                    Frag gl = ld_frag8(&S.fB.Am[1][wm + m16][ko]);
+                    Frag d0 = ld_frag8(&S.fB.Bs[wn + m16][ko]);
+                    Frag d1 = ld_frag8(&S.fB.Bs[wn + 16 + m16][ko]);
+                    acc[0] = mfma16(gh, d0, acc[0]);
+                    acc[0] = mfma16(gl, d0, acc[0]);
+                    acc[1] = mfma16(gh, d1, acc[1]);
+                    acc[1] = mfma16(gl, d1, acc[1]);
+                }
+            }
+            S.fB.zred[ra][tid & 7] = zacc;
+            __syncthreads();
+            if (tid < 32) {
+                float s = ((S.fB.zred[tid][0] + S.fB.zred[tid][1]) + (S.fB.zred[tid][2] + S.fB.zred[tid][3]))
+                        + ((S.fB.zred[tid][4] + S.fB.zred[tid][5]) + (S.fB.zred[tid][6] + S.fB.zred[tid][7]));
+                S.fB.Zl[tid] = 1.0f / s;
+            }
+            __syncthreads();
+            {
+                float zv[2][4];
+#pragma unroll
+                for (int j = 0; j < 2; ++j)
+#pragma unroll
+                    for (int rr = 0; rr < 4; ++rr) {
+                        int m = wm + quad * 4 + rr;
+                        zv[j][rr] = acc[j][rr] * S.fB.Zl[m];
+                    }
+                __syncthreads();
+#pragma unroll
+                for (int j = 0; j < 2; ++j)
+#pragma unroll
+                    for (int rr = 0; rr < 4; ++rr) {
+                        int m = wm + quad * 4 + rr;
+                        int d = wn + j * 16 + m16;
+                        S.fB.Am[0][m][d] = bf16_rne(zv[j][rr]);
+                    }
+            }
+            __syncthreads();
+#pragma unroll
+            for (int t = 0; t < 8; ++t) {
+                const int n0 = wave * 128 + t * 16;
+                Frag bf0 = ld_frag8(&wofh[(size_t)(n0 + m16) * 768 + 512 + h * 64 + quad * 8]);
+                Frag bf1 = ld_frag8(&wofh[(size_t)(n0 + m16) * 768 + 512 + h * 64 + 32 + quad * 8]);
+#pragma unroll
+                for (int qi = 0; qi < 2; ++qi) {
+                    Frag za = ld_frag8(&S.fB.Am[0][qi * 16 + m16][quad * 8]);
+                    Frag zb = ld_frag8(&S.fB.Am[0][qi * 16 + m16][32 + quad * 8]);
+                    floatx4 ac = (floatx4){0.f, 0.f, 0.f, 0.f};
+                    ac = mfma16(za, bf0, ac);
+                    ac = mfma16(zb, bf1, ac);
+#pragma unroll
+                    for (int rr = 0; rr < 4; ++rr) {
+                        int m = b * T_ + q0 + qi * 16 + quad * 4 + rr;
+                        unsafeAtomicAdd(&out[(size_t)m * 512 + n0 + m16], ac[rr]);
+                    }
+                }
             }
         }
     }
@@ -642,13 +637,13 @@
     u16* wah    = (u16*)(ws + 3342336);
     float* rs1  = ws + 3670016;
     float* rt1  = ws + 4259840;
-
-    prep_kernel<<<1216, 256, 0, stream>>>(x, ln1_g, ln1_b, ln2_g, ln2_b,
-                                          x1h, x2h,
-                                          Wqkv, wqh, Wabcde, wah,
-                                          Wo, Wp, wofh, rs1, out);
-    gemm_dual<<<dim3(44, 12), 256, 0, stream>>>(x1h, wqh, x2h, wah,
-                                                babcde, qkv, proj);
-    attn_tritt<<<96 + 1536, 256, 0, stream>>>(qkv, proj, aoh, rs1, rt1);
-    finale<<<288, 256, 0, stream>>>(aoh, rs1, rt1, proj, wofh, bo, bp, out);
-}
+    u32* bar    = (u32*)(ws + 4849664);
+
+    hipMemsetAsync(bar, 0, sizeof(u32), stream);
+    mega<<<GRID_, 256, 0, stream>>>(x, ln1_g, ln1_b, ln2_g, ln2_b,
+                                    Wqkv, Wabcde, Wo, Wp,
+                                    babcde, bo, bp,
+                                    proj, wofh, aoh, qkv,
+                                    x1h, x2h, wqh, wah,
+                                    rs1, rt1, bar, out);
+}
```

New measurement: 329.4 us. 2.36x slower.
